# Optimization experiments

Hardware: AMD Instinct MI355X
Metric: run time of the kernel (lower is better)

Reference implementation:

```python
import jax, jax.numpy as jnp
import numpy as np
from jax import lax

B, T, CD, HD, VD, QD = 2048, 20, 512, 1024, 2048, 1024

def leaky(x):
    return jax.nn.leaky_relu(x, negative_slope=0.01)

def gru_cell(x, h, w_ih, w_hh, b_ih, b_hh):
    # torch.nn.GRUCell math
    gi = x @ w_ih.T + b_ih            # [B, 3H]
    gh = h @ w_hh.T + b_hh            # [B, 3H]
    i_r, i_z, i_n = jnp.split(gi, 3, axis=-1)
    h_r, h_z, h_n = jnp.split(gh, 3, axis=-1)
    r = jax.nn.sigmoid(i_r + h_r)
    z = jax.nn.sigmoid(i_z + h_z)
    n = jnp.tanh(i_n + r * h_n)
    return (1.0 - z) * n + z * h


def setup_inputs() -> dict:
    key = jax.random.key(0)
    ks = jax.random.split(key, 16)
    s = 0.05
    return {
        "v": jax.random.normal(ks[0], (B, VD), dtype=jnp.float32),
        "q": jax.random.normal(ks[1], (B, QD), dtype=jnp.float32),
        "caption": jax.random.normal(ks[2], (B, T, CD), dtype=jnp.float32),
        "cap_len": jax.random.randint(ks[3], (B,), 0, T),
        # word_rnn: GRUCell(c_dim -> c_dim)
        "w_ih1": jax.random.normal(ks[4], (3 * CD, CD), dtype=jnp.float32) * s,
        "w_hh1": jax.random.normal(ks[5], (3 * CD, CD), dtype=jnp.float32) * s,
        "b_ih1": jax.random.normal(ks[6], (3 * CD,), dtype=jnp.float32) * s,
        "b_hh1": jax.random.normal(ks[7], (3 * CD,), dtype=jnp.float32) * s,
        # caption_rnn: GRUCell(c_dim -> hidden_dim)
        "w_ih2": jax.random.normal(ks[8], (3 * HD, CD), dtype=jnp.float32) * s,
        "w_hh2": jax.random.normal(ks[9], (3 * HD, HD), dtype=jnp.float32) * s,
        "b_ih2": jax.random.normal(ks[10], (3 * HD,), dtype=jnp.float32) * s,
        "b_hh2": jax.random.normal(ks[11], (3 * HD,), dtype=jnp.float32) * s,
        # attention: W_v Linear(v_dim -> c_dim, no bias), W_q Linear(q_dim -> c_dim, no bias)
        "Wv": jax.random.normal(ks[12], (CD, VD), dtype=jnp.float32) * s,
        "Wq": jax.random.normal(ks[13], (CD, QD), dtype=jnp.float32) * s,
        # fcnet: Linear(hidden_dim -> hidden_dim, no bias)
        "Wfc": jax.random.normal(ks[14], (HD, HD), dtype=jnp.float32) * s,
    }


def reference(v, q, caption, cap_len, w_ih1, w_hh1, b_ih1, b_hh1,
              w_ih2, w_hh2, b_ih2, b_hh2, Wv, Wq, Wfc):
    # Dropout is inference-mode identity. Sorting by length + restore_id is
    # equivalent to full-batch masked processing in original order.
    b = caption.shape[0]
    fv = leaky(v @ Wv.T)              # [B, c_dim] attention visual projection
    fq = leaky(q @ Wq.T)              # [B, c_dim]
    cap_t = jnp.transpose(caption, (1, 0, 2))  # [T, B, c_dim]

    h1_0 = jnp.zeros((b, CD), caption.dtype)
    h2_0 = jnp.zeros((b, HD), caption.dtype)

    def step(carry, inputs):
        h1, h2 = carry
        x_t, t = inputs
        active = (t < cap_len)[:, None]           # rows still inside their caption
        h1n = gru_cell(x_t, h1, w_ih1, w_hh1, b_ih1, b_hh1)
        h1 = jnp.where(active, h1n, h1)
        att = jax.nn.sigmoid(h1 * fv + h1 * fq) * x_t   # [B, c_dim]
        h2n = gru_cell(att, h2, w_ih2, w_hh2, b_ih2, b_hh2)
        h2 = jnp.where(active, h2n, h2)
        out_t = jnp.where(active, leaky(h2 @ Wfc.T), 0.0)  # [B, hidden]
        a_t = jnp.where(active, att, 0.0)                  # [B, c_dim]
        return (h1, h2), (out_t, a_t)

    (_, _), (outs, alphas) = lax.scan(step, (h1_0, h2_0),
                                      (cap_t, jnp.arange(T)))
    # MaxPool1d over the time axis of [B, hidden, T] (zeros at padded steps)
    output = jnp.max(outs, axis=0)               # [B, hidden]
    alphas = jnp.transpose(alphas, (1, 0, 2))    # [B, T, c_dim]
    return output, alphas
```

## Files before the change

### kernel.cpp

```cpp
#include <hip/hip_runtime.h>

typedef _Float16 half_t;
typedef half_t half8 __attribute__((ext_vector_type(8)));
typedef half_t half4 __attribute__((ext_vector_type(4)));
typedef float  floatx4 __attribute__((ext_vector_type(4)));

#define NB 2048
#define NT 20
#define CD 512
#define HD 1024
#define VD 2048
#define QD 1024


__device__ __forceinline__ float sigmoidf_(float x) { return 1.0f / (1.0f + __expf(-x)); }
__device__ __forceinline__ float tanhf_(float x)    { return 1.0f - 2.0f / (1.0f + __expf(2.0f * x)); }
__device__ __forceinline__ float lrelu_(float x)    { return x > 0.0f ? x : 0.01f * x; }

__device__ __forceinline__ void gload16(const half_t* g, half_t* l) {
    __builtin_amdgcn_global_load_lds(
        (const __attribute__((address_space(1))) void*)g,
        (__attribute__((address_space(3))) void*)l, 16, 0, 0);
}

__device__ __forceinline__ void remap(int flat, int GX, int& m0, int& c0) {
    const int xcd = flat & 7;
    const int i   = flat >> 3;
    c0 = (xcd * (GX >> 3) + (i >> 5)) * 32;
    m0 = (i & 31) * 64;
}

template <int NG, int BN, int NACC,
          int I0A, int I1A, int I2A, int I0B, int I1B, int I2B>
__device__ __forceinline__ void gemm2(
    const half_t* __restrict__ A1, int lda1, const half_t* __restrict__ W1, long gs1, int S1,
    const half_t* __restrict__ A2, int lda2, const half_t* __restrict__ W2, long gs2, int S2,
    int m0, int c0, half_t* lds, floatx4 (&acc)[NACC][2][BN / 32])
{
    constexpr int ASZ = 64 * 64;
    constexpr int WL  = (NG * BN * 8) / 256;
    constexpr int BUF = ASZ + NG * BN * 64;
    constexpr int NIN = BN / 32;
    constexpr int map_[3] = {I0A, I1A, I2A};
    constexpr int mapB[3] = {I0B, I1B, I2B};

    const int tid  = threadIdx.x;
    const int lane = tid & 63;
    const int wid  = tid >> 6;
    const int wr   = (wid >> 1) * 32;
    const int wc   = (wid & 1) * (BN / 2);
    const int frow = lane & 15;
    const int cb   = lane >> 4;

    const int srow = tid >> 3;
    const int sq   = ((tid & 7) ^ (srow & 7)) * 8;
    const int sdl  = srow * 64 + (tid & 7) * 8;
    const long aoff1 = (long)(m0 + srow) * lda1 + sq;
    const long aoff2 = (long)(m0 + srow) * lda2 + sq;

    int  wdst[WL];
    long woff1[WL], woff2[WL];
#pragma unroll
    for (int j = 0; j < WL; ++j) {
        const int u   = tid + j * 256;
        const int g   = u / (BN * 8);
        const int idx = u - g * (BN * 8);
        const int row = idx >> 3;
        const int q   = ((idx & 7) ^ (row & 7)) * 8;
        wdst[j]  = ASZ + u * 8;
        woff1[j] = (long)g * gs1 + (long)(c0 + row) * (S1 * 64) + q;
        woff2[j] = (long)g * gs2 + (long)(c0 + row) * (S2 * 64) + q;
    }

    const int S = S1 + S2;
    auto stage = [&](int s, int buf) {
        half_t* lb = lds + buf * BUF;
        if (s < S1) {
            const int k0 = s * 64;
            gload16(A1 + aoff1 + k0,             lb + sdl);
            gload16(A1 + aoff1 + 32 * lda1 + k0, lb + 32 * 64 + sdl);
#pragma unroll
            for (int j = 0; j < WL; ++j) gload16(W1 + woff1[j] + k0, lb + wdst[j]);
        } else {
            const int k0 = (s - S1) * 64;
            gload16(A2 + aoff2 + k0,             lb + sdl);
            gload16(A2 + aoff2 + 32 * lda2 + k0, lb + 32 * 64 + sdl);
#pragma unroll
            for (int j = 0; j < WL; ++j) gload16(W2 + woff2[j] + k0, lb + wdst[j]);
        }
    };

    stage(0, 0);
    __syncthreads();
    int cur = 0;
    for (int s = 0; s < S; ++s) {
        if (s + 1 < S) stage(s + 1, cur ^ 1);
        const half_t* lb = lds + cur * BUF;
        const bool pa = (s < S1);
#pragma unroll
        for (int kk = 0; kk < 2; ++kk) {
            half8 af[2];
#pragma unroll
            for (int im = 0; im < 2; ++im) {
                const int r = wr + im * 16 + frow;
                af[im] = *(const half8*)(lb + r * 64 + (((kk * 4 + cb) ^ (r & 7)) * 8));
            }
#pragma unroll
            for (int g = 0; g < NG; ++g) {
#pragma unroll
                for (int in = 0; in < NIN; ++in) {
                    const int r = wc + in * 16 + frow;
                    const half8 bf = *(const half8*)(lb + ASZ + g * (BN * 64) + r * 64 +
                                                     (((kk * 4 + cb) ^ (r & 7)) * 8));
                    const int d = pa ? map_[g] : mapB[g];
#pragma unroll
                    for (int im = 0; im < 2; ++im)
                        acc[d][im][in] = __builtin_amdgcn_mfma_f32_16x16x32_f16(
                            af[im], bf, acc[d][im][in], 0, 0, 0);
                }
            }
        }
        __syncthreads();
        cur ^= 1;
    }
}

__global__ void sort_kernel(const int* __restrict__ cap_len,
                            int* __restrict__ perm, int* __restrict__ cnt)
{
    __shared__ int hist[NT];
    __shared__ int off[NT];
    const int tid = threadIdx.x;
    if (tid < NT) hist[tid] = 0;
    __syncthreads();
    for (int i = tid; i < NB; i += 256) atomicAdd(&hist[cap_len[i]], 1);
    __syncthreads();
    if (tid == 0) {
        int run = 0;
        for (int v = NT - 1; v >= 0; --v) { off[v] = run; run += hist[v]; }
        for (int t = 0; t < NT; ++t) cnt[t] = off[t];
        for (int t = NT; t < 32; ++t) cnt[t] = 0;
    }
    __syncthreads();
    for (int i = tid; i < NB; i += 256) {
        const int pos = atomicAdd(&off[cap_len[i]], 1);
        perm[pos] = i;
    }
}

struct CvtArgs {
    const float* src[10];
    half_t* dst[10];
    int start[11];
    int rowlen[10];
    const int* perm;
    const int* cnt;
};
__global__ void cvt_all_kernel(CvtArgs a) {
    const int b = blockIdx.x;
    int i = 0;
#pragma unroll
    for (int k = 0; k < 9; ++k) i += (b >= a.start[k + 1]);
    const int idx = ((b - a.start[i]) * 256 + (int)threadIdx.x) * 4;
    long sidx = idx;
    const int rl = a.rowlen[i];
    if (rl) {
        const int row = idx / rl;
        if (row >= a.cnt[0]) return;
        sidx = (long)a.perm[row] * rl + (idx - row * rl);
    }
    float4 f = *(const float4*)(a.src[i] + sidx);
    half4 h = {(half_t)f.x, (half_t)f.y, (half_t)f.z, (half_t)f.w};
    *(half4*)(a.dst[i] + idx) = h;
}


__device__ __forceinline__ void step1_body(
    int flat,
    const half_t* __restrict__ cap_h,
    const half_t* __restrict__ wih1, const half_t* __restrict__ whh1,
    const float* __restrict__ b_ih1, const float* __restrict__ b_hh1,
    const half_t* __restrict__ h1_src, half_t* __restrict__ h1_dst,
    const float* __restrict__ fvq, const float* __restrict__ caption,
    const int* __restrict__ perm, int cn,
    half_t* __restrict__ att_w, float* __restrict__ alphas, int t, half_t* lds)
{
    int m0, c0; remap(flat, 16, m0, c0);
    if (m0 >= cn) return;
    floatx4 acc[4][2][1];
#pragma unroll
    for (int g = 0; g < 4; ++g) for (int im = 0; im < 2; ++im)
        acc[g][im][0] = (floatx4){0.f, 0.f, 0.f, 0.f};
    gemm2<3, 32, 4, 0, 1, 2, 0, 1, 3>(
        cap_h + t * CD, NT * CD, wih1, (long)CD * CD, CD / 64,
        h1_src, CD, whh1, (long)CD * CD, CD / 64, m0, c0, lds, acc);

    const int lane = threadIdx.x & 63;
    const int wid = threadIdx.x >> 6;
    const int wr = (wid >> 1) * 32, wc = (wid & 1) * 16;
#pragma unroll
    for (int im = 0; im < 2; ++im) {
        const int mb = m0 + wr + im * 16 + (lane >> 4) * 4;
        const int c  = c0 + wc + (lane & 15);
        const float br = b_ih1[c] + b_hh1[c];
        const float bz = b_ih1[CD + c] + b_hh1[CD + c];
        const float bin_ = b_ih1[2 * CD + c];
        const float bhn  = b_hh1[2 * CD + c];
#pragma unroll
        for (int j = 0; j < 4; ++j) {
            const int m = mb + j;
            const float r = sigmoidf_(acc[0][im][0][j] + br);
            const float z = sigmoidf_(acc[1][im][0][j] + bz);
            const float n = tanhf_(acc[2][im][0][j] + bin_ + r * (acc[3][im][0][j] + bhn));
            const float h_old = (float)h1_src[m * CD + c];
            const bool act = m < cn;
            const float h_new = act ? ((1.f - z) * n + z * h_old) : h_old;
            const int orig = perm[m];
            const float x = caption[((long)orig * NT + t) * CD + c];
            const float at = sigmoidf_(h_new * fvq[m * CD + c]) * x;
            h1_dst[m * CD + c] = (half_t)h_new;
            att_w[m * CD + c]  = (half_t)at;
            if (act) alphas[((long)orig * NT + t) * CD + c] = at;
        }
    }
}

__device__ __forceinline__ void step2_body(
    int flat,
    const half_t* __restrict__ att_r,
    const half_t* __restrict__ wih2, const half_t* __restrict__ whh2,
    const float* __restrict__ b_ih2, const float* __restrict__ b_hh2,
    const half_t* __restrict__ h2_src, half_t* __restrict__ h2_dst,
    int cn, int t, half_t* lds)
{
    int m0, c0; remap(flat, 32, m0, c0);
    if (m0 >= cn) return;
    floatx4 acc[4][2][1];
#pragma unroll
    for (int g = 0; g < 4; ++g) for (int im = 0; im < 2; ++im)
        acc[g][im][0] = (floatx4){0.f, 0.f, 0.f, 0.f};
    gemm2<3, 32, 4, 0, 1, 2, 0, 1, 3>(
        att_r, CD, wih2, (long)HD * CD, CD / 64,
        h2_src, HD, whh2, (long)HD * HD, HD / 64, m0, c0, lds, acc);

    const int lane = threadIdx.x & 63;
    const int wid = threadIdx.x >> 6;
    const int wr = (wid >> 1) * 32, wc = (wid & 1) * 16;
#pragma unroll
    for (int im = 0; im < 2; ++im) {
        const int mb = m0 + wr + im * 16 + (lane >> 4) * 4;
        const int c  = c0 + wc + (lane & 15);
        const float br = b_ih2[c] + b_hh2[c];
        const float bz = b_ih2[HD + c] + b_hh2[HD + c];
        const float bin_ = b_ih2[2 * HD + c];
        const float bhn  = b_hh2[2 * HD + c];
#pragma unroll
        for (int j = 0; j < 4; ++j) {
            const int m = mb + j;
            const float r = sigmoidf_(acc[0][im][0][j] + br);
            const float z = sigmoidf_(acc[1][im][0][j] + bz);
            const float n = tanhf_(acc[2][im][0][j] + bin_ + r * (acc[3][im][0][j] + bhn));
            const float h_old = (float)h2_src[m * HD + c];
            const bool act = m < cn;
            h2_dst[m * HD + c] = (half_t)(act ? ((1.f - z) * n + z * h_old) : h_old);
        }
    }
}

__device__ __forceinline__ void step3_body(
    int flat,
    const half_t* __restrict__ h2_cur, const half_t* __restrict__ wfc,
    const int* __restrict__ perm, int cn,
    float* __restrict__ outmax, half_t* lds)
{
    int m0, c0; remap(flat, 32, m0, c0);
    if (m0 >= cn) return;
    floatx4 acc[1][2][1];
#pragma unroll
    for (int im = 0; im < 2; ++im)
        acc[0][im][0] = (floatx4){0.f, 0.f, 0.f, 0.f};
    gemm2<1, 32, 1, 0, 0, 0, 0, 0, 0>(
        h2_cur, HD, wfc, 0, HD / 64,
        h2_cur, HD, wfc, 0, 0, m0, c0, lds, acc);

    const int lane = threadIdx.x & 63;
    const int wid = threadIdx.x >> 6;
    const int wr = (wid >> 1) * 32, wc = (wid & 1) * 16;
#pragma unroll
    for (int im = 0; im < 2; ++im) {
        const int mb = m0 + wr + im * 16 + (lane >> 4) * 4;
        const int c  = c0 + wc + (lane & 15);
#pragma unroll
        for (int j = 0; j < 4; ++j) {
            const int m = mb + j;
            if (m < cn) {
                const int orig = perm[m];
                const float v0 = lrelu_(acc[0][im][0][j]);
                float* p = &outmax[(long)orig * HD + c];
                *p = fmaxf(*p, v0);
            }
        }
    }
}

__global__ __launch_bounds__(256, 4) void step1_0_kernel(
    const half_t* __restrict__ v_h, const half_t* __restrict__ wv_w,
    const half_t* __restrict__ q_h, const half_t* __restrict__ wq_w,
    const half_t* __restrict__ cap_h, const half_t* __restrict__ wih1,
    const float* __restrict__ b_ih1, const float* __restrict__ b_hh1,
    half_t* __restrict__ h1_dst, float* __restrict__ fvq_out,
    const float* __restrict__ caption, const int* __restrict__ perm,
    const int* __restrict__ cnt,
    half_t* __restrict__ att_w, float* __restrict__ alphas)
{
    __shared__ half_t lds[2 * (64 * 64 + 3 * 32 * 64)];
    const int cn = cnt[0];
    int m0, c0; remap(blockIdx.x, 16, m0, c0);
    if (m0 >= cn) return;

    floatx4 acc1[2][2][1];
#pragma unroll
    for (int g = 0; g < 2; ++g) for (int im = 0; im < 2; ++im)
        acc1[g][im][0] = (floatx4){0.f, 0.f, 0.f, 0.f};
    gemm2<1, 32, 2, 0, 0, 0, 1, 0, 0>(
        v_h, VD, wv_w, 0, VD / 64, q_h, QD, wq_w, 0, QD / 64, m0, c0, lds, acc1);

    floatx4 acc2[3][2][1];
#pragma unroll
    for (int g = 0; g < 3; ++g) for (int im = 0; im < 2; ++im)
        acc2[g][im][0] = (floatx4){0.f, 0.f, 0.f, 0.f};
    gemm2<3, 32, 3, 0, 1, 2, 0, 1, 2>(
        cap_h, NT * CD, wih1, (long)CD * CD, CD / 64,
        cap_h, NT * CD, wih1, (long)CD * CD, 0, m0, c0, lds, acc2);

    const int lane = threadIdx.x & 63;
    const int wid = threadIdx.x >> 6;
    const int wr = (wid >> 1) * 32, wc = (wid & 1) * 16;
#pragma unroll
    for (int im = 0; im < 2; ++im) {
        const int mb = m0 + wr + im * 16 + (lane >> 4) * 4;
        const int c  = c0 + wc + (lane & 15);
        const float br = b_ih1[c] + b_hh1[c];
        const float bz = b_ih1[CD + c] + b_hh1[CD + c];
        const float bin_ = b_ih1[2 * CD + c];
        const float bhn  = b_hh1[2 * CD + c];
#pragma unroll
        for (int j = 0; j < 4; ++j) {
            const int m = mb + j;
            const float fv = lrelu_(acc1[0][im][0][j]) + lrelu_(acc1[1][im][0][j]);
            fvq_out[m * CD + c] = fv;
            const float r = sigmoidf_(acc2[0][im][0][j] + br);
            const float z = sigmoidf_(acc2[1][im][0][j] + bz);
            const float n = tanhf_(acc2[2][im][0][j] + bin_ + r * bhn);
            const bool act = m < cn;
            const float h_new = act ? (1.f - z) * n : 0.f;
            const int orig = perm[m];
            const float x = caption[(long)orig * NT * CD + c];
            const float at = sigmoidf_(h_new * fv) * x;
            h1_dst[m * CD + c] = (half_t)h_new;
            att_w[m * CD + c]  = (half_t)at;
            if (act) alphas[(long)orig * NT * CD + c] = at;
        }
    }
}

__global__ __launch_bounds__(256, 4) void fused321_kernel(
    const half_t* __restrict__ att0, half_t* __restrict__ att1,
    const half_t* __restrict__ wih2, const half_t* __restrict__ whh2,
    const float* __restrict__ b_ih2, const float* __restrict__ b_hh2,
    const half_t* __restrict__ h2b0, half_t* __restrict__ h2b1,
    const half_t* __restrict__ cap_h,
    const half_t* __restrict__ wih1, const half_t* __restrict__ whh1,
    const float* __restrict__ b_ih1, const float* __restrict__ b_hh1,
    const half_t* __restrict__ h1b0, half_t* __restrict__ h1b1,
    const float* __restrict__ fvq, const float* __restrict__ caption,
    const half_t* __restrict__ wfc,
    const int* __restrict__ perm, const int* __restrict__ cnt,
    float* __restrict__ outmax, float* __restrict__ alphas, int t)
{
    __shared__ half_t lds[2 * (64 * 64 + 3 * 32 * 64)];
    const int par = t & 1;
    const half_t* att_r = par ? att1 : att0;
    half_t*       att_w = par ? (half_t*)att0 : att1;
    const half_t* h2_r  = par ? h2b1 : h2b0;
    half_t*       h2_w  = par ? (half_t*)h2b0 : h2b1;
    const half_t* h1_r  = par ? h1b0 : h1b1;
    half_t*       h1_w  = par ? h1b1 : (half_t*)h1b0;

    const int bx = blockIdx.x;
    if (bx < 1024) {
        if (t < NT)
            step2_body(bx, att_r, wih2, whh2, b_ih2, b_hh2, h2_r, h2_w,
                       cnt[t], t, lds);
    } else if (bx < 1536) {
        if (t < NT - 1)
            step1_body(bx - 1024, cap_h, wih1, whh1, b_ih1, b_hh1,
                       h1_r, h1_w, fvq, caption, perm, cnt[t + 1],
                       att_w, alphas, t + 1, lds);
    } else {
        if (t >= 1)
            step3_body(bx - 1536, h2_r, wfc, perm, cnt[t - 1], outmax, lds);
    }
}

extern "C" void kernel_launch(void* const* d_in, const int* in_sizes, int n_in,
                              void* d_out, int out_size, void* d_ws, size_t ws_size,
                              hipStream_t stream)
{
    (void)in_sizes; (void)n_in; (void)out_size; (void)ws_size;
    const float* v     = (const float*)d_in[0];
    const float* q     = (const float*)d_in[1];
    const float* cap   = (const float*)d_in[2];
    const int*   cap_len = (const int*)d_in[3];
    const float* w_ih1 = (const float*)d_in[4];
    const float* w_hh1 = (const float*)d_in[5];
    const float* b_ih1 = (const float*)d_in[6];
    const float* b_hh1 = (const float*)d_in[7];
    const float* w_ih2 = (const float*)d_in[8];
    const float* w_hh2 = (const float*)d_in[9];
    const float* b_ih2 = (const float*)d_in[10];
    const float* b_hh2 = (const float*)d_in[11];
    const float* Wv    = (const float*)d_in[12];
    const float* Wq    = (const float*)d_in[13];
    const float* Wfc   = (const float*)d_in[14];

    float* out_max = (float*)d_out;
    float* alphas  = (float*)d_out + (size_t)NB * HD;

    half_t* p = (half_t*)d_ws;
    half_t* v_h    = p; p += (size_t)NB * VD;
    half_t* q_h    = p; p += (size_t)NB * QD;
    half_t* cap_h  = p; p += (size_t)NB * NT * CD;
    half_t* wih1_h = p; p += 3 * CD * CD;
    half_t* whh1_h = p; p += 3 * CD * CD;
    half_t* wih2_h = p; p += 3 * HD * CD;
    half_t* whh2_h = p; p += 3 * HD * HD;
    half_t* wfc_h  = p; p += HD * HD;
    half_t* wv_h   = p; p += CD * VD;
    half_t* wq_h   = p; p += CD * QD;
    half_t* h1b0   = p; p += (size_t)NB * CD;
    half_t* h1b1   = p; p += (size_t)NB * CD;
    half_t* h2b0   = p; p += (size_t)NB * HD;
    half_t* h2b1   = p; p += (size_t)NB * HD;
    half_t* att0   = p; p += (size_t)NB * CD;
    half_t* att1   = p; p += (size_t)NB * CD;
    float* fvq = (float*)p; p += (size_t)NB * CD * 2;
    int* perm = (int*)p;
    int* cnt  = perm + NB;

    hipMemsetAsync(out_max, 0, (size_t)NB * HD * sizeof(float), stream);
    hipMemsetAsync(alphas, 0, (size_t)NB * NT * CD * sizeof(float), stream);
    hipMemsetAsync(h2b0, 0, (size_t)NB * HD * sizeof(half_t), stream);

    sort_kernel<<<1, 256, 0, stream>>>(cap_len, perm, cnt);

    CvtArgs ca;
    const float* srcs[10] = {v, q, cap, w_ih1, w_hh1, w_ih2, w_hh2, Wfc, Wv, Wq};
    half_t* dsts[10] = {v_h, q_h, cap_h, wih1_h, whh1_h, wih2_h, whh2_h, wfc_h, wv_h, wq_h};
    const int ns[10] = {NB * VD, NB * QD, NB * NT * CD, 3 * CD * CD, 3 * CD * CD,
                        3 * HD * CD, 3 * HD * HD, HD * HD, CD * VD, CD * QD};
    const int rls[10] = {VD, QD, NT * CD, 0, 0, 0, 0, 0, 0, 0};
    int acc_blk = 0;
    for (int i = 0; i < 10; ++i) {
        ca.src[i] = srcs[i]; ca.dst[i] = dsts[i]; ca.rowlen[i] = rls[i];
        ca.start[i] = acc_blk; acc_blk += ns[i] / 1024;
    }
    ca.start[10] = acc_blk;
    ca.perm = perm; ca.cnt = cnt;
    cvt_all_kernel<<<acc_blk, 256, 0, stream>>>(ca);

    step1_0_kernel<<<512, 256, 0, stream>>>(
        v_h, wv_h, q_h, wq_h, cap_h, wih1_h, b_ih1, b_hh1,
        h1b1, fvq, cap, perm, cnt, att0, alphas);

    for (int t = 0; t <= NT; ++t) {
        fused321_kernel<<<2560, 256, 0, stream>>>(
            att0, att1, wih2_h, whh2_h, b_ih2, b_hh2, h2b0, h2b1,
            cap_h, wih1_h, whh1_h, b_ih1, b_hh1, h1b0, h1b1,
            fvq, cap, wfc_h, perm, cnt, out_max, alphas, t);
    }
}
```

Measured before the change: 966.2 us.

## Triple-buffer GEMM LDS pipeline with explicit vmcnt waits and single barrier

Changes the shared GEMM mainloop from double to triple buffering, prefetching two K-stages ahead and using explicit s_waitcnt vmcnt plus one s_barrier per iteration instead of two __syncthreads. This aims to hide global-to-LDS load latency and cut barrier overhead. LDS per block grows by half and launch bounds drop from 4 to 2 blocks per CU, reducing occupancy.

```diff
diff --git a/kernel.cpp b/kernel.cpp
--- a/kernel.cpp
+++ b/kernel.cpp
@@ -17,6 +17,13 @@
 __device__ __forceinline__ float tanhf_(float x)    { return 1.0f - 2.0f / (1.0f + __expf(2.0f * x)); }
 __device__ __forceinline__ float lrelu_(float x)    { return x > 0.0f ? x : 0.01f * x; }
 
+template <int N> __device__ __forceinline__ void waitv() {
+    asm volatile("s_waitcnt vmcnt(%0)" :: "n"(N) : "memory");
+}
+__device__ __forceinline__ void barrier_() {
+    asm volatile("s_barrier" ::: "memory");
+}
+
 __device__ __forceinline__ void gload16(const half_t* g, half_t* l) {
     __builtin_amdgcn_global_load_lds(
         (const __attribute__((address_space(1))) void*)g,
@@ -40,6 +47,7 @@
     constexpr int ASZ = 64 * 64;
     constexpr int WL  = (NG * BN * 8) / 256;
     constexpr int BUF = ASZ + NG * BN * 64;
+    constexpr int LPT = 2 + WL;
     constexpr int NIN = BN / 32;
     constexpr int map_[3] = {I0A, I1A, I2A};
     constexpr int mapB[3] = {I0B, I1B, I2B};
@@ -73,8 +81,7 @@
     }
 
     const int S = S1 + S2;
-    auto stage = [&](int s, int buf) {
-        half_t* lb = lds + buf * BUF;
+    auto stage = [&](int s, half_t* lb) {
         if (s < S1) {
             const int k0 = s * 64;
             gload16(A1 + aoff1 + k0,             lb + sdl);
@@ -90,12 +97,20 @@
         }
     };
 
-    stage(0, 0);
-    __syncthreads();
-    int cur = 0;
+    half_t* b0 = lds;
+    half_t* b1 = lds + BUF;
+    half_t* b2 = lds + 2 * BUF;
+    stage(0, b0);
+    if (S > 1) stage(1, b1);
+    half_t* pc = b0;
+    half_t* pn = b1;
+    half_t* ps = b2;
+
     for (int s = 0; s < S; ++s) {
-        if (s + 1 < S) stage(s + 1, cur ^ 1);
-        const half_t* lb = lds + cur * BUF;
+        if (s + 1 < S) waitv<LPT>(); else waitv<0>();
+        barrier_();
+        if (s + 2 < S) stage(s + 2, ps);
+        const half_t* lb = pc;
         const bool pa = (s < S1);
 #pragma unroll
         for (int kk = 0; kk < 2; ++kk) {
@@ -120,9 +135,9 @@
                 }
             }
         }
-        __syncthreads();
-        cur ^= 1;
-    }
+        half_t* tp = pc; pc = pn; pn = ps; ps = tp;
+    }
+    barrier_();
 }
 
 __global__ void sort_kernel(const int* __restrict__ cap_len,
@@ -303,7 +318,7 @@
     }
 }
 
-__global__ __launch_bounds__(256, 4) void step1_0_kernel(
+__global__ __launch_bounds__(256, 2) void step1_0_kernel(
     const half_t* __restrict__ v_h, const half_t* __restrict__ wv_w,
     const half_t* __restrict__ q_h, const half_t* __restrict__ wq_w,
     const half_t* __restrict__ cap_h, const half_t* __restrict__ wih1,
@@ -313,7 +328,7 @@
     const int* __restrict__ cnt,
     half_t* __restrict__ att_w, float* __restrict__ alphas)
 {
-    __shared__ half_t lds[2 * (64 * 64 + 3 * 32 * 64)];
+    __shared__ half_t lds[3 * (64 * 64 + 3 * 32 * 64)];
     const int cn = cnt[0];
     int m0, c0; remap(blockIdx.x, 16, m0, c0);
     if (m0 >= cn) return;
@@ -364,7 +379,7 @@
     }
 }
 
-__global__ __launch_bounds__(256, 4) void fused321_kernel(
+__global__ __launch_bounds__(256, 2) void fused321_kernel(
     const half_t* __restrict__ att0, half_t* __restrict__ att1,
     const half_t* __restrict__ wih2, const half_t* __restrict__ whh2,
     const float* __restrict__ b_ih2, const float* __restrict__ b_hh2,
@@ -378,7 +393,7 @@
     const int* __restrict__ perm, const int* __restrict__ cnt,
     float* __restrict__ outmax, float* __restrict__ alphas, int t)
 {
-    __shared__ half_t lds[2 * (64 * 64 + 3 * 32 * 64)];
+    __shared__ half_t lds[3 * (64 * 64 + 3 * 32 * 64)];
     const int par = t & 1;
     const half_t* att_r = par ? att1 : att0;
     half_t*       att_w = par ? (half_t*)att0 : att1;
```

Measured after the change: 967.1 us. No clear change (+0.1%).

## Double GEMM row tile to 128 with 512-thread blocks

Applied to the files above, without the earlier changes.

Block tiles grow from 64 to 128 batch rows and blocks from 256 to 512 threads (8 waves). Each weight tile loaded into LDS is therefore reused by twice as many rows, halving weight traffic per output. Grid sizes and the block-index ranges in the fused step kernel shrink to match. The cost is larger LDS per block, fewer blocks per CU, and coarser early-exit granularity for rows past the active caption count.

```diff
diff --git a/kernel.cpp b/kernel.cpp
--- a/kernel.cpp
+++ b/kernel.cpp
@@ -26,21 +26,20 @@
 __device__ __forceinline__ void remap(int flat, int GX, int& m0, int& c0) {
     const int xcd = flat & 7;
     const int i   = flat >> 3;
-    c0 = (xcd * (GX >> 3) + (i >> 5)) * 32;
-    m0 = (i & 31) * 64;
-}
-
-template <int NG, int BN, int NACC,
+    c0 = (xcd * (GX >> 3) + (i >> 4)) * 32;
+    m0 = (i & 15) * 128;
+}
+
+template <int NG, int NACC,
           int I0A, int I1A, int I2A, int I0B, int I1B, int I2B>
 __device__ __forceinline__ void gemm2(
     const half_t* __restrict__ A1, int lda1, const half_t* __restrict__ W1, long gs1, int S1,
     const half_t* __restrict__ A2, int lda2, const half_t* __restrict__ W2, long gs2, int S2,
-    int m0, int c0, half_t* lds, floatx4 (&acc)[NACC][2][BN / 32])
-{
-    constexpr int ASZ = 64 * 64;
-    constexpr int WL  = (NG * BN * 8) / 256;
-    constexpr int BUF = ASZ + NG * BN * 64;
-    constexpr int NIN = BN / 32;
+    int m0, int c0, half_t* lds, floatx4 (&acc)[NACC][2][1])
+{
+    constexpr int ASZ = 128 * 64;
+    constexpr int WCH = NG * 256;
+    constexpr int BUF = ASZ + NG * 2048;
     constexpr int map_[3] = {I0A, I1A, I2A};
     constexpr int mapB[3] = {I0B, I1B, I2B};
 
@@ -48,28 +47,34 @@
     const int lane = tid & 63;
     const int wid  = tid >> 6;
     const int wr   = (wid >> 1) * 32;
-    const int wc   = (wid & 1) * (BN / 2);
+    const int wc   = (wid & 1) * 16;
     const int frow = lane & 15;
     const int cb   = lane >> 4;
 
-    const int srow = tid >> 3;
-    const int sq   = ((tid & 7) ^ (srow & 7)) * 8;
-    const int sdl  = srow * 64 + (tid & 7) * 8;
-    const long aoff1 = (long)(m0 + srow) * lda1 + sq;
-    const long aoff2 = (long)(m0 + srow) * lda2 + sq;
-
-    int  wdst[WL];
-    long woff1[WL], woff2[WL];
-#pragma unroll
-    for (int j = 0; j < WL; ++j) {
-        const int u   = tid + j * 256;
-        const int g   = u / (BN * 8);
-        const int idx = u - g * (BN * 8);
-        const int row = idx >> 3;
-        const int q   = ((idx & 7) ^ (row & 7)) * 8;
-        wdst[j]  = ASZ + u * 8;
-        woff1[j] = (long)g * gs1 + (long)(c0 + row) * (S1 * 64) + q;
-        woff2[j] = (long)g * gs2 + (long)(c0 + row) * (S2 * 64) + q;
+    const int arow = tid >> 3;
+    const int aq   = ((tid & 7) ^ (arow & 7)) * 8;
+    const int adst = arow * 64 + (tid & 7) * 8;
+    const long aof1 = (long)(m0 + arow) * lda1 + aq;
+    const long aof2 = (long)(m0 + arow) * lda2 + aq;
+
+    const bool w0v = tid < WCH;
+    const bool w1v = tid + 512 < WCH;
+    int wdst0, wdst1; long wof10, wof11, wof20, wof21;
+    {
+        const int u = tid;
+        const int g = u >> 8, idx = u & 255, row = idx >> 3, ch = idx & 7;
+        const int q = (ch ^ (row & 7)) * 8;
+        wdst0 = ASZ + u * 8;
+        wof10 = (long)g * gs1 + (long)(c0 + row) * (S1 * 64) + q;
+        wof20 = (long)g * gs2 + (long)(c0 + row) * (S2 * 64) + q;
+    }
+    {
+        const int u = tid + 512;
+        const int g = u >> 8, idx = u & 255, row = idx >> 3, ch = idx & 7;
+        const int q = (ch ^ (row & 7)) * 8;
+        wdst1 = ASZ + u * 8;
+        wof11 = (long)g * gs1 + (long)(c0 + row) * (S1 * 64) + q;
+        wof21 = (long)g * gs2 + (long)(c0 + row) * (S2 * 64) + q;
     }
 
     const int S = S1 + S2;
@@ -77,16 +82,16 @@
         half_t* lb = lds + buf * BUF;
         if (s < S1) {
             const int k0 = s * 64;
-            gload16(A1 + aoff1 + k0,             lb + sdl);
-            gload16(A1 + aoff1 + 32 * lda1 + k0, lb + 32 * 64 + sdl);
-#pragma unroll
-            for (int j = 0; j < WL; ++j) gload16(W1 + woff1[j] + k0, lb + wdst[j]);
+            gload16(A1 + aof1 + k0,             lb + adst);
+            gload16(A1 + aof1 + 64 * lda1 + k0, lb + adst + 64 * 64);
+            if (w0v) gload16(W1 + wof10 + k0, lb + wdst0);
+            if (w1v) gload16(W1 + wof11 + k0, lb + wdst1);
         } else {
             const int k0 = (s - S1) * 64;
-            gload16(A2 + aoff2 + k0,             lb + sdl);
-            gload16(A2 + aoff2 + 32 * lda2 + k0, lb + 32 * 64 + sdl);
-#pragma unroll
-            for (int j = 0; j < WL; ++j) gload16(W2 + woff2[j] + k0, lb + wdst[j]);
+            gload16(A2 + aof2 + k0,             lb + adst);
+            gload16(A2 + aof2 + 64 * lda2 + k0, lb + adst + 64 * 64);
+            if (w0v) gload16(W2 + wof20 + k0, lb + wdst0);
+            if (w1v) gload16(W2 + wof21 + k0, lb + wdst1);
         }
     };
 
@@ -107,17 +112,14 @@
             }
 #pragma unroll
             for (int g = 0; g < NG; ++g) {
-#pragma unroll
-                for (int in = 0; in < NIN; ++in) {
-                    const int r = wc + in * 16 + frow;
-                    const half8 bf = *(const half8*)(lb + ASZ + g * (BN * 64) + r * 64 +
-                                                     (((kk * 4 + cb) ^ (r & 7)) * 8));
-                    const int d = pa ? map_[g] : mapB[g];
-#pragma unroll
-                    for (int im = 0; im < 2; ++im)
-                        acc[d][im][in] = __builtin_amdgcn_mfma_f32_16x16x32_f16(
-                            af[im], bf, acc[d][im][in], 0, 0, 0);
-                }
+                const int r = wc + frow;
+                const half8 bf = *(const half8*)(lb + ASZ + g * 2048 + r * 64 +
+                                                 (((kk * 4 + cb) ^ (r & 7)) * 8));
+                const int d = pa ? map_[g] : mapB[g];
+#pragma unroll
+                for (int im = 0; im < 2; ++im)
+                    acc[d][im][0] = __builtin_amdgcn_mfma_f32_16x16x32_f16(
+                        af[im], bf, acc[d][im][0], 0, 0, 0);
             }
         }
         __syncthreads();
@@ -191,7 +193,7 @@
 #pragma unroll
     for (int g = 0; g < 4; ++g) for (int im = 0; im < 2; ++im)
         acc[g][im][0] = (floatx4){0.f, 0.f, 0.f, 0.f};
-    gemm2<3, 32, 4, 0, 1, 2, 0, 1, 3>(
+    gemm2<3, 4, 0, 1, 2, 0, 1, 3>(
         cap_h + t * CD, NT * CD, wih1, (long)CD * CD, CD / 64,
         h1_src, CD, whh1, (long)CD * CD, CD / 64, m0, c0, lds, acc);
 
@@ -239,7 +241,7 @@
 #pragma unroll
     for (int g = 0; g < 4; ++g) for (int im = 0; im < 2; ++im)
         acc[g][im][0] = (floatx4){0.f, 0.f, 0.f, 0.f};
-    gemm2<3, 32, 4, 0, 1, 2, 0, 1, 3>(
+    gemm2<3, 4, 0, 1, 2, 0, 1, 3>(
         att_r, CD, wih2, (long)HD * CD, CD / 64,
         h2_src, HD, whh2, (long)HD * HD, HD / 64, m0, c0, lds, acc);
 
@@ -279,7 +281,7 @@
 #pragma unroll
     for (int im = 0; im < 2; ++im)
         acc[0][im][0] = (floatx4){0.f, 0.f, 0.f, 0.f};
-    gemm2<1, 32, 1, 0, 0, 0, 0, 0, 0>(
+    gemm2<1, 1, 0, 0, 0, 0, 0, 0>(
         h2_cur, HD, wfc, 0, HD / 64,
         h2_cur, HD, wfc, 0, 0, m0, c0, lds, acc);
 
@@ -303,7 +305,7 @@
     }
 }
 
-__global__ __launch_bounds__(256, 4) void step1_0_kernel(
+__global__ __launch_bounds__(512, 4) void step1_0_kernel(
     const half_t* __restrict__ v_h, const half_t* __restrict__ wv_w,
     const half_t* __restrict__ q_h, const half_t* __restrict__ wq_w,
     const half_t* __restrict__ cap_h, const half_t* __restrict__ wih1,
@@ -313,7 +315,7 @@
     const int* __restrict__ cnt,
     half_t* __restrict__ att_w, float* __restrict__ alphas)
 {
-    __shared__ half_t lds[2 * (64 * 64 + 3 * 32 * 64)];
+    __shared__ half_t lds[2 * (128 * 64 + 3 * 2048)];
     const int cn = cnt[0];
     int m0, c0; remap(blockIdx.x, 16, m0, c0);
     if (m0 >= cn) return;
@@ -322,14 +324,14 @@
 #pragma unroll
     for (int g = 0; g < 2; ++g) for (int im = 0; im < 2; ++im)
         acc1[g][im][0] = (floatx4){0.f, 0.f, 0.f, 0.f};
-    gemm2<1, 32, 2, 0, 0, 0, 1, 0, 0>(
+    gemm2<1, 2, 0, 0, 0, 1, 0, 0>(
         v_h, VD, wv_w, 0, VD / 64, q_h, QD, wq_w, 0, QD / 64, m0, c0, lds, acc1);
 
     floatx4 acc2[3][2][1];
 #pragma unroll
     for (int g = 0; g < 3; ++g) for (int im = 0; im < 2; ++im)
         acc2[g][im][0] = (floatx4){0.f, 0.f, 0.f, 0.f};
-    gemm2<3, 32, 3, 0, 1, 2, 0, 1, 2>(
+    gemm2<3, 3, 0, 1, 2, 0, 1, 2>(
         cap_h, NT * CD, wih1, (long)CD * CD, CD / 64,
         cap_h, NT * CD, wih1, (long)CD * CD, 0, m0, c0, lds, acc2);
 
@@ -364,7 +366,7 @@
     }
 }
 
-__global__ __launch_bounds__(256, 4) void fused321_kernel(
+__global__ __launch_bounds__(512, 4) void fused321_kernel(
     const half_t* __restrict__ att0, half_t* __restrict__ att1,
     const half_t* __restrict__ wih2, const half_t* __restrict__ whh2,
     const float* __restrict__ b_ih2, const float* __restrict__ b_hh2,
@@ -378,7 +380,7 @@
     const int* __restrict__ perm, const int* __restrict__ cnt,
     float* __restrict__ outmax, float* __restrict__ alphas, int t)
 {
-    __shared__ half_t lds[2 * (64 * 64 + 3 * 32 * 64)];
+    __shared__ half_t lds[2 * (128 * 64 + 3 * 2048)];
     const int par = t & 1;
     const half_t* att_r = par ? att1 : att0;
     half_t*       att_w = par ? (half_t*)att0 : att1;
@@ -388,18 +390,18 @@
     half_t*       h1_w  = par ? h1b1 : (half_t*)h1b0;
 
     const int bx = blockIdx.x;
-    if (bx < 1024) {
+    if (bx < 512) {
         if (t < NT)
             step2_body(bx, att_r, wih2, whh2, b_ih2, b_hh2, h2_r, h2_w,
                        cnt[t], t, lds);
-    } else if (bx < 1536) {
+    } else if (bx < 768) {
         if (t < NT - 1)
-            step1_body(bx - 1024, cap_h, wih1, whh1, b_ih1, b_hh1,
+            step1_body(bx - 512, cap_h, wih1, whh1, b_ih1, b_hh1,
                        h1_r, h1_w, fvq, caption, perm, cnt[t + 1],
                        att_w, alphas, t + 1, lds);
     } else {
         if (t >= 1)
-            step3_body(bx - 1536, h2_r, wfc, perm, cnt[t - 1], outmax, lds);
+            step3_body(bx - 768, h2_r, wfc, perm, cnt[t - 1], outmax, lds);
     }
 }
 
@@ -469,12 +471,12 @@
     ca.perm = perm; ca.cnt = cnt;
     cvt_all_kernel<<<acc_blk, 256, 0, stream>>>(ca);
 
-    step1_0_kernel<<<512, 256, 0, stream>>>(
+    step1_0_kernel<<<256, 512, 0, stream>>>(
         v_h, wv_h, q_h, wq_h, cap_h, wih1_h, b_ih1, b_hh1,
         h1b1, fvq, cap, perm, cnt, att0, alphas);
 
     for (int t = 0; t <= NT; ++t) {
-        fused321_kernel<<<2560, 256, 0, stream>>>(
+        fused321_kernel<<<1280, 512, 0, stream>>>(
             att0, att1, wih2_h, whh2_h, b_ih2, b_hh2, h2b0, h2b1,
             cap_h, wih1_h, whh1_h, b_ih1, b_hh1, h1b0, h1b1,
             fvq, cap, wfc_h, perm, cnt, out_max, alphas, t);
```

Result: no change. 973.9 us (+0.8%).
